# Kernel tuning notes

Measured on AMD Instinct MI355X. Metric: run time of the kernel, lower is better.

The kernel has to match this reference:

```python
import jax, jax.numpy as jnp
import numpy as np

N, DIM, RF_DIM, H, W, PN, TOPK = 16, 2048, 256, 16, 8, 64, 10  # TOPK = 2*k = 2*(K//2)


def conv1x1(w, x):
    # w: [O, C] (1x1 conv kernel), x: [b, C, h, w] -> [b, O, h, w]
    return jnp.einsum('oc,bchw->bohw', w, x)


def calibration(x, y):
    # x, y: [b, c, h, w]
    b, c, h, w = x.shape
    xv = x.reshape(b, c, h * w)
    yv = y.reshape(b, c, h * w)
    c_aff = jax.nn.softmax(jnp.einsum('bcm,bdm->bcd', xv, yv), axis=2)  # [b,c,c]
    s_aff = jax.nn.softmax(jnp.einsum('bcm,bcn->bmn', xv, yv), axis=2)  # [b,hw,hw]
    c_avg = c_aff.mean(axis=-1)  # [b,c]
    s_avg = s_aff.mean(axis=-1)  # [b,hw]
    aff = (c_avg[:, :, None] * s_avg[:, None, :]).reshape(b, c, h, w)
    pos = jax.nn.relu(aff - 0.5) + 0.5
    comp = jax.nn.relu(0.5 - aff) + 0.5
    return x * pos + y * comp


def instance_norm(x, eps=1e-5):
    m = x.mean(axis=(2, 3), keepdims=True)
    v = x.var(axis=(2, 3), keepdims=True)
    return (x - m) * jax.lax.rsqrt(v + eps)


def setup_inputs():
    key = jax.random.key(0)
    ks = jax.random.split(key, 6)
    return {
        'inputs': jax.random.normal(ks[0], (N, DIM, H, W), jnp.float32),
        'mv_prototype': jax.random.normal(ks[1], (PN, DIM, H, W), jnp.float32),
        'w_rf': jax.random.normal(ks[2], (RF_DIM, DIM), jnp.float32) * 0.02,
        'w_rf_mv': jax.random.normal(ks[3], (DIM, TOPK * RF_DIM), jnp.float32) * 0.02,
        'w_rm_s': jax.random.normal(ks[4], (DIM, DIM), jnp.float32) * 0.02,
        'w_fuse': jax.random.normal(ks[5], (DIM, DIM), jnp.float32) * 0.02,
    }


def reference(inputs, mv_prototype, w_rf, w_rf_mv, w_rm_s, w_fuse):
    n, c, h, w = inputs.shape
    # pairwise squared euclidean distance (addmm-style cdist)
    xf = inputs.reshape(n, -1)
    pf = mv_prototype.reshape(mv_prototype.shape[0], -1)
    dist = (xf * xf).sum(1, keepdims=True) + (pf * pf).sum(1)[None, :] - 2.0 * xf @ pf.T
    idx = jnp.argsort(dist, axis=1)[:, :TOPK]  # [n, 2k] nearest prototypes
    # refine prototypes then gather per-sample top-2k and stack channels
    xp = conv1x1(w_rf, mv_prototype)  # [pn, rf_dim, h, w]
    mv_list = xp[idx].reshape(n, TOPK * RF_DIM, h, w)
    mvl = conv1x1(w_rf_mv, mv_list)  # [n, dim, h, w]
    mvl = jax.nn.relu(calibration(inputs, mvl))
    mv_a = instance_norm(conv1x1(w_rm_s, mvl))
    x_fuse = jax.nn.sigmoid(conv1x1(w_fuse, mv_a))
    return inputs + inputs * x_fuse
```

## Files before the change

kernel.cpp:

```cpp
#include <hip/hip_runtime.h>
#include <cstdint>
#include <cstddef>

#define N_    16
#define DIM_  2048
#define RF_   256
#define PN_   64
#define TOPK_ 10
#define HW_   128
#define KFULL (DIM_*HW_)
#define KMV   (TOPK_*RF_)

#define AS1 __attribute__((address_space(1)))
#define AS3 __attribute__((address_space(3)))

typedef __attribute__((ext_vector_type(8))) short bf16x8;
typedef __attribute__((ext_vector_type(4))) float f32x4;
typedef __attribute__((ext_vector_type(8))) unsigned short u16x8;

__device__ __forceinline__ unsigned short f2bf(float f) {
  unsigned u = __builtin_bit_cast(unsigned, f);
  unsigned r = (u + 0x7FFFu + ((u >> 16) & 1u)) >> 16;
  return (unsigned short)r;
}

__global__ __launch_bounds__(256)
void cvt_all_kernel(const float* __restrict__ s0, const float* __restrict__ s1,
                    const float* __restrict__ s2, const float* __restrict__ s3,
                    unsigned short* __restrict__ d0, unsigned short* __restrict__ d1,
                    unsigned short* __restrict__ d2, unsigned short* __restrict__ d3,
                    float* __restrict__ dsum) {
  __shared__ u16x8 tile[32][65];
  const int t = threadIdx.x;
  int gid = blockIdx.x * 256 + t;
  if (gid < 1152) dsum[gid] = 0.f;

  int bid = blockIdx.x;
  const float* s; unsigned short* d; int O, CG, tb;
  if (bid < 32)       { s = s0; d = d0; O = RF_;  CG = DIM_ / 8; tb = bid; }
  else if (bid < 352) { s = s1; d = d1; O = DIM_; CG = KMV  / 8; tb = bid - 32; }
  else if (bid < 608) { s = s2; d = d2; O = DIM_; CG = DIM_ / 8; tb = bid - 352; }
  else                { s = s3; d = d3; O = DIM_; CG = DIM_ / 8; tb = bid - 608; }
  const int nCgT = CG / 32;
  const int o0  = (tb / nCgT) * 64;
  const int cg0 = (tb % nCgT) * 32;
  const size_t C = (size_t)CG * 8;

#pragma unroll
  for (int i = 0; i < 8; ++i) {
    int idx = i * 256 + t, ol = idx >> 5, cg = idx & 31;
    const float* sp = s + (size_t)(o0 + ol) * C + (size_t)(cg0 + cg) * 8;
    float4 a = *(const float4*)sp;
    float4 b = *(const float4*)(sp + 4);
    u16x8 pk;
    pk[0] = f2bf(a.x); pk[1] = f2bf(a.y); pk[2] = f2bf(a.z); pk[3] = f2bf(a.w);
    pk[4] = f2bf(b.x); pk[5] = f2bf(b.y); pk[6] = f2bf(b.z); pk[7] = f2bf(b.w);
    tile[cg][ol] = pk;
  }
  __syncthreads();
#pragma unroll
  for (int i = 0; i < 8; ++i) {
    int idx = i * 256 + t, cg = idx >> 6, ol = idx & 63;
    *(u16x8*)(d + (size_t)(cg0 + cg) * ((size_t)O * 8) + (size_t)(o0 + ol) * 8) =
        tile[cg][ol];
  }
}

__global__ __launch_bounds__(256)
void transpose_proto_kernel(const float* __restrict__ src,
                            unsigned short* __restrict__ dst,
                            float* __restrict__ pnorm_part) {
  __shared__ float tile[32][129];
  __shared__ float ssq[4];
  const int p = blockIdx.x;
  const int c0 = blockIdx.y * 32;
  const int t = threadIdx.x;
  const float* sp = src + ((size_t)p * DIM_ + c0) * HW_;
  float sq = 0.f;
#pragma unroll
  for (int i = 0; i < 4; ++i) {
    int g = i * 256 + t;
    int ci = g >> 5, s4 = g & 31;
    float4 v = *(const float4*)(sp + (size_t)ci * HW_ + s4 * 4);
    sq += v.x * v.x + v.y * v.y + v.z * v.z + v.w * v.w;
    int sb = s4 * 4;
    tile[ci][sb] = v.x; tile[ci][sb + 1] = v.y; tile[ci][sb + 2] = v.z; tile[ci][sb + 3] = v.w;
  }
#pragma unroll
  for (int m = 1; m < 64; m <<= 1) sq += __shfl_xor(sq, m, 64);
  if ((t & 63) == 0) ssq[t >> 6] = sq;
  __syncthreads();
  if (t == 0) pnorm_part[blockIdx.y * PN_ + p] = ssq[0] + ssq[1] + ssq[2] + ssq[3];
  unsigned short* dp = dst + (size_t)p * HW_ * DIM_ + (size_t)(c0 >> 3) * 1024;
#pragma unroll
  for (int i = 0; i < 2; ++i) {
    int cidx = i * 256 + t;
    int kg = cidx >> 7, s = cidx & 127;
    u16x8 pk;
#pragma unroll
    for (int u = 0; u < 8; ++u) pk[u] = f2bf(tile[kg * 8 + u][s]);
    *(u16x8*)(dp + (size_t)kg * 1024 + (size_t)s * 8) = pk;
  }
}

__global__ __launch_bounds__(256)
void dist_partial_kernel(const float* __restrict__ x, const float* __restrict__ proto,
                         float* __restrict__ part) {
  __shared__ alignas(16) float xl[2][16][68];
  __shared__ alignas(16) float pl[2][64][68];
  const int t = threadIdx.x, b = blockIdx.x;
  const int n0 = t & 7, pb = t >> 3;
  const int xr = t >> 4, xc = (t & 15) * 4;
  float acc[2][2] = {};
  const size_t kbase = (size_t)b * 512;

  float4 rx, rp[4];
  auto gload = [&](int ph) {
    const size_t k0 = kbase + ph * 64;
    rx = *(const float4*)(x + (size_t)xr * KFULL + k0 + xc);
#pragma unroll
    for (int i = 0; i < 4; ++i) {
      int idx = i * 256 + t;
      rp[i] = *(const float4*)(proto + (size_t)(idx >> 4) * KFULL + k0 + (idx & 15) * 4);
    }
  };
  auto swrite = [&](int buf) {
    *(float4*)&xl[buf][xr][xc] = rx;
#pragma unroll
    for (int i = 0; i < 4; ++i) {
      int idx = i * 256 + t;
      *(float4*)&pl[buf][idx >> 4][(idx & 15) * 4] = rp[i];
    }
  };

  gload(0); swrite(0);
  __syncthreads();
  for (int ph = 0; ph < 8; ++ph) {
    const int buf = ph & 1;
    if (ph + 1 < 8) gload(ph + 1);
#pragma unroll 8
    for (int k = 0; k < 64; k += 4) {
      float4 xa = *(float4*)&xl[buf][n0][k];
      float4 xb = *(float4*)&xl[buf][n0 + 8][k];
      float4 p0 = *(float4*)&pl[buf][pb][k];
      float4 p1 = *(float4*)&pl[buf][pb + 32][k];
      acc[0][0] += xa.x*p0.x + xa.y*p0.y + xa.z*p0.z + xa.w*p0.w;
      acc[0][1] += xa.x*p1.x + xa.y*p1.y + xa.z*p1.z + xa.w*p1.w;
      acc[1][0] += xb.x*p0.x + xb.y*p0.y + xb.z*p0.z + xb.w*p0.w;
      acc[1][1] += xb.x*p1.x + xb.y*p1.y + xb.z*p1.z + xb.w*p1.w;
    }
    if (ph + 1 < 8) swrite(buf ^ 1);
    __syncthreads();
  }

  float* scratch = (float*)xl;
  scratch[n0 * 64 + pb]            = -2.f * acc[0][0];
  scratch[n0 * 64 + pb + 32]       = -2.f * acc[0][1];
  scratch[(n0 + 8) * 64 + pb]      = -2.f * acc[1][0];
  scratch[(n0 + 8) * 64 + pb + 32] = -2.f * acc[1][1];
  __syncthreads();
  *(float4*)(part + (size_t)b * 1024 + t * 4) = *(const float4*)&scratch[t * 4];
}

__global__ __launch_bounds__(512)
void select_kernel(const float* __restrict__ part, const float* __restrict__ pnorm_part,
                   int* __restrict__ idx, int* __restrict__ flags) {
  __shared__ float red[8][64];
  __shared__ float sh[64];
  const int n = blockIdx.x, t = threadIdx.x;
  const int c = t & 63, ch = t >> 6;
  const float* pp = part + (size_t)ch * 64 * 1024 + n * 64 + c;
  float a0 = 0.f, a1 = 0.f, a2 = 0.f, a3 = 0.f;
  for (int b = 0; b < 64; b += 4) {
    a0 += pp[(size_t)(b + 0) * 1024];
    a1 += pp[(size_t)(b + 1) * 1024];
    a2 += pp[(size_t)(b + 2) * 1024];
    a3 += pp[(size_t)(b + 3) * 1024];
  }
  red[ch][c] = (a0 + a1) + (a2 + a3);
  __syncthreads();
  if (t < 64) {
    float pn = 0.f;
#pragma unroll 8
    for (int cb = 0; cb < DIM_ / 32; ++cb) pn += pnorm_part[cb * PN_ + t];
    float dv = pn;
#pragma unroll
    for (int i = 0; i < 8; ++i) dv += red[i][t];
    sh[t] = dv;
  }
  __syncthreads();
  if (t < 64) {
    float dval = sh[t];
    int rank = 0;
#pragma unroll
    for (int j = 0; j < 64; ++j) {
      float o = sh[j];
      rank += (o < dval || (o == dval && j < t)) ? 1 : 0;
    }
    if (rank < TOPK_) { idx[n * TOPK_ + rank] = t; flags[t] = 1; }
  }
}

#define BM 64
#define BKK 64

template <int MODE>
__global__ __launch_bounds__(256, 2)
void mfma_gemm_kernel(const unsigned short* __restrict__ Wb,
                      const unsigned short* __restrict__ Xb,
                      void* __restrict__ OutP,
                      const float* __restrict__ inputs,
                      const int* __restrict__ idxp,
                      const int* __restrict__ flags,
                      int K, int O, int Ldim) {
  __shared__ alignas(16) unsigned short Al[3][8 * BM * 8];
  __shared__ alignas(16) unsigned short Bl[3][8 * 128 * 8];

  const int t = threadIdx.x;
  const int w = t >> 6;
  const int lane = t & 63;
  const int q = lane >> 4;
  const int l15 = lane & 15;
  const int m2 = w >> 1;
  const int h  = w & 1;
  const int batch = blockIdx.y;
  const int o0 = blockIdx.x * BM;

  if (MODE == 0 && flags && !flags[batch]) return;

  int idreg = 0;
  if (MODE == 1 && lane < TOPK_) idreg = idxp[batch * TOPK_ + lane];

  f32x4 acc[2][4] = {};

  auto issue = [&](int k0, int buf) {
#pragma unroll
    for (int i = 0; i < 2; ++i) {
      int qk = w * 2 + i;
      const unsigned short* ga =
          Wb + (size_t)((k0 >> 3) + qk) * (O * 8) + (size_t)(o0 + lane) * 8;
      __builtin_amdgcn_global_load_lds((const AS1 void*)ga,
                                       (AS3 void*)(&Al[buf][qk * 512]), 16, 0, 0);
    }
    const unsigned short* base;
    if (MODE == 1) {
      int id = __shfl(idreg, k0 >> 8, 64);
      base = Xb + (size_t)id * (HW_ * RF_) + (size_t)((k0 & 255) >> 3) * 1024;
    } else {
      base = Xb + (size_t)batch * HW_ * K + (size_t)(k0 >> 3) * 1024;
    }
#pragma unroll
    for (int i = 0; i < 4; ++i) {
      int v = w * 4 + i;
      int qk = v >> 1, hh = v & 1;
      const unsigned short* gb = base + (size_t)qk * 1024 + (size_t)(hh * 64 + lane) * 8;
      __builtin_amdgcn_global_load_lds((const AS1 void*)gb,
                                       (AS3 void*)(&Bl[buf][qk * 1024 + hh * 512]), 16, 0, 0);
    }
  };

  const int nIter = K / BKK;

  issue(0, 0);
  issue(BKK, 1);

  for (int it = 0; it < nIter; ++it) {
    const int buf = it % 3;
    if (it + 1 < nIter) {
      asm volatile("s_waitcnt vmcnt(6)" ::: "memory");
    } else {
      asm volatile("s_waitcnt vmcnt(0)" ::: "memory");
    }
    __builtin_amdgcn_s_barrier();
#pragma unroll
    for (int s = 0; s < 2; ++s) {
      bf16x8 af[2], bfr[4];
#pragma unroll
      for (int mt = 0; mt < 2; ++mt)
        af[mt] = *(const bf16x8*)(&Al[buf][(s * 4 + q) * 512 + (m2 * 32 + mt * 16 + l15) * 8]);
#pragma unroll
      for (int nt = 0; nt < 4; ++nt)
        bfr[nt] = *(const bf16x8*)(&Bl[buf][(s * 4 + q) * 1024 + (h * 64 + nt * 16 + l15) * 8]);
#pragma unroll
      for (int mt = 0; mt < 2; ++mt)
#pragma unroll
        for (int nt = 0; nt < 4; ++nt)
          acc[mt][nt] = __builtin_amdgcn_mfma_f32_16x16x32_bf16(af[mt], bfr[nt], acc[mt][nt], 0, 0, 0);
    }
    if (it + 2 < nIter) issue((it + 2) * BKK, (it + 2) % 3);
  }

  const float CAL = 1.0f - 1.0f / 262144.0f;

  float* nsumS = (float*)&Al[0][0];
  float* nsqS  = (float*)&Al[0][0] + 128;

  if (MODE == 2) {
#pragma unroll
    for (int mt = 0; mt < 2; ++mt)
#pragma unroll
      for (int reg = 0; reg < 4; ++reg) {
        float s_ = 0.f, q_ = 0.f;
#pragma unroll
        for (int nt = 0; nt < 4; ++nt) {
          float v = acc[mt][nt][reg];
          s_ += v; q_ += v * v;
        }
#pragma unroll
        for (int m = 1; m < 16; m <<= 1) {
          s_ += __shfl_xor(s_, m, 64);
          q_ += __shfl_xor(q_, m, 64);
        }
        if (l15 == 0) {
          int ol = mt * 16 + q * 4 + reg;
          nsumS[w * 32 + ol] = s_; nsqS[w * 32 + ol] = q_;
        }
      }
    __syncthreads();
  }

  if (MODE == 3) {
    float* ofb = (float*)OutP + (size_t)batch * DIM_ * HW_;
    const float* inb = inputs + (size_t)batch * DIM_ * HW_;
#pragma unroll
    for (int mt = 0; mt < 2; ++mt)
#pragma unroll
      for (int nt = 0; nt < 4; ++nt) {
        int o = o0 + m2 * 32 + mt * 16 + q * 4;
        int s = h * 64 + nt * 16 + l15;
        f32x4 v = acc[mt][nt];
#pragma unroll
        for (int g = 0; g < 4; ++g) {
          float in = inb[(size_t)(o + g) * HW_ + s];
          float sg = 1.f / (1.f + expf(-v[g]));
          ofb[(size_t)(o + g) * HW_ + s] = in * (1.f + sg);
        }
      }
  } else {
    unsigned short* ob = (unsigned short*)OutP + (size_t)batch * HW_ * Ldim;
    const float* inb = (MODE == 1) ? inputs + (size_t)batch * DIM_ * HW_ : nullptr;
#pragma unroll
    for (int mt = 0; mt < 2; ++mt) {
      float mean[4], rs[4];
      if (MODE == 2) {
#pragma unroll
        for (int reg = 0; reg < 4; ++reg) {
          int ol = mt * 16 + q * 4 + reg;
          float ts = nsumS[(m2 * 2 + 0) * 32 + ol] + nsumS[(m2 * 2 + 1) * 32 + ol];
          float tq = nsqS[(m2 * 2 + 0) * 32 + ol] + nsqS[(m2 * 2 + 1) * 32 + ol];
          float mn = ts * (1.f / 128.f);
          float vr = tq * (1.f / 128.f) - mn * mn;
          mean[reg] = mn; rs[reg] = rsqrtf(vr + 1e-5f);
        }
      }
#pragma unroll
      for (int nt = 0; nt < 4; ++nt) {
        int o = o0 + m2 * 32 + mt * 16 + q * 4;
        int s = h * 64 + nt * 16 + l15;
        f32x4 v = acc[mt][nt];
        float r[4];
        if (MODE == 0) {
#pragma unroll
          for (int g = 0; g < 4; ++g) r[g] = v[g];
        } else if (MODE == 1) {
          const float* ip = inb + (size_t)o * HW_ + s;
#pragma unroll
          for (int g = 0; g < 4; ++g)
            r[g] = fmaxf(0.f, 0.5f * ip[(size_t)g * HW_] + CAL * v[g]);
        } else {
#pragma unroll
          for (int g = 0; g < 4; ++g) r[g] = (v[g] - mean[g]) * rs[g];
        }
        ushort4 pk;
        pk.x = f2bf(r[0]); pk.y = f2bf(r[1]); pk.z = f2bf(r[2]); pk.w = f2bf(r[3]);
        *(ushort4*)(ob + (size_t)(o >> 3) * 1024 + (size_t)s * 8 + (o & 7)) = pk;
      }
    }
  }
}

extern "C" void kernel_launch(void* const* d_in, const int* in_sizes, int n_in,
                              void* d_out, int out_size, void* d_ws, size_t ws_size,
                              hipStream_t stream) {
  const float* inputs = (const float*)d_in[0];
  const float* proto  = (const float*)d_in[1];
  const float* w_rf   = (const float*)d_in[2];
  const float* w_rfmv = (const float*)d_in[3];
  const float* w_rms  = (const float*)d_in[4];
  const float* w_fuse = (const float*)d_in[5];
  float* out = (float*)d_out;

  uint8_t* ws = (uint8_t*)d_ws;
  size_t off = 0;
  auto alloc = [&](size_t bytes) { uint8_t* p = ws + off; off += (bytes + 255) & ~(size_t)255; return p; };

  float* dsum  = (float*)alloc(1088 * 4);
  int*   flags = (int*)alloc(PN_ * 4);
  int*   idx   = (int*)alloc(N_ * TOPK_ * 4);
  float* pnorm = (float*)alloc((size_t)(DIM_ / 32) * PN_ * 4);
  float* part  = (float*)alloc((size_t)512 * 1024 * 4);
  unsigned short* wrf_b   = (unsigned short*)alloc((size_t)RF_ * DIM_ * 2);
  unsigned short* wrfmv_b = (unsigned short*)alloc((size_t)DIM_ * KMV * 2);
  unsigned short* wrms_b  = (unsigned short*)alloc((size_t)DIM_ * DIM_ * 2);
  unsigned short* wfuse_b = (unsigned short*)alloc((size_t)DIM_ * DIM_ * 2);
  unsigned short* xpT     = (unsigned short*)alloc((size_t)PN_ * HW_ * RF_ * 2);
  unsigned short* protoT  = (unsigned short*)alloc((size_t)PN_ * HW_ * DIM_ * 2);
  unsigned short* mvlT = protoT;
  unsigned short* mvaT = protoT + (size_t)N_ * HW_ * DIM_;

  cvt_all_kernel<<<864, 256, 0, stream>>>(w_rf, w_rfmv, w_rms, w_fuse,
                                          wrf_b, wrfmv_b, wrms_b, wfuse_b, dsum);
  transpose_proto_kernel<<<dim3(PN_, DIM_ / 32), 256, 0, stream>>>(proto, protoT, pnorm);
  dist_partial_kernel<<<512, 256, 0, stream>>>(inputs, proto, part);
  select_kernel<<<N_, 512, 0, stream>>>(part, pnorm, idx, flags);

  mfma_gemm_kernel<0><<<dim3(RF_ / BM, PN_), 256, 0, stream>>>(
      wrf_b, protoT, xpT, nullptr, nullptr, flags, DIM_, RF_, RF_);
  mfma_gemm_kernel<1><<<dim3(DIM_ / BM, N_), 256, 0, stream>>>(
      wrfmv_b, xpT, mvlT, inputs, idx, nullptr, KMV, DIM_, DIM_);
  mfma_gemm_kernel<2><<<dim3(DIM_ / BM, N_), 256, 0, stream>>>(
      wrms_b, mvlT, mvaT, nullptr, nullptr, nullptr, DIM_, DIM_, DIM_);
  mfma_gemm_kernel<3><<<dim3(DIM_ / BM, N_), 256, 0, stream>>>(
      wfuse_b, mvaT, out, inputs, nullptr, nullptr, DIM_, DIM_, DIM_);
}
```

Baseline: 316.4 us.

## Merge front-end kernels into one launch and widen GEMM blocks to 512 threads

```diff
diff --git a/kernel.cpp b/kernel.cpp
--- a/kernel.cpp
+++ b/kernel.cpp
@@ -25,141 +25,143 @@
 }
 
 __global__ __launch_bounds__(256)
-void cvt_all_kernel(const float* __restrict__ s0, const float* __restrict__ s1,
-                    const float* __restrict__ s2, const float* __restrict__ s3,
-                    unsigned short* __restrict__ d0, unsigned short* __restrict__ d1,
-                    unsigned short* __restrict__ d2, unsigned short* __restrict__ d3,
-                    float* __restrict__ dsum) {
-  __shared__ u16x8 tile[32][65];
+void front_kernel(const float* __restrict__ x, const float* __restrict__ proto,
+                  float* __restrict__ part,
+                  unsigned short* __restrict__ protoT, float* __restrict__ pnorm_part,
+                  const float* __restrict__ s0, const float* __restrict__ s1,
+                  const float* __restrict__ s2, const float* __restrict__ s3,
+                  unsigned short* __restrict__ d0, unsigned short* __restrict__ d1,
+                  unsigned short* __restrict__ d2, unsigned short* __restrict__ d3,
+                  float* __restrict__ dsum) {
+  __shared__ alignas(16) unsigned char ldsbuf[43520];
   const int t = threadIdx.x;
-  int gid = blockIdx.x * 256 + t;
-  if (gid < 1152) dsum[gid] = 0.f;
-
-  int bid = blockIdx.x;
-  const float* s; unsigned short* d; int O, CG, tb;
-  if (bid < 32)       { s = s0; d = d0; O = RF_;  CG = DIM_ / 8; tb = bid; }
-  else if (bid < 352) { s = s1; d = d1; O = DIM_; CG = KMV  / 8; tb = bid - 32; }
-  else if (bid < 608) { s = s2; d = d2; O = DIM_; CG = DIM_ / 8; tb = bid - 352; }
-  else                { s = s3; d = d3; O = DIM_; CG = DIM_ / 8; tb = bid - 608; }
-  const int nCgT = CG / 32;
-  const int o0  = (tb / nCgT) * 64;
-  const int cg0 = (tb % nCgT) * 32;
-  const size_t C = (size_t)CG * 8;
-
-#pragma unroll
-  for (int i = 0; i < 8; ++i) {
-    int idx = i * 256 + t, ol = idx >> 5, cg = idx & 31;
-    const float* sp = s + (size_t)(o0 + ol) * C + (size_t)(cg0 + cg) * 8;
-    float4 a = *(const float4*)sp;
-    float4 b = *(const float4*)(sp + 4);
-    u16x8 pk;
-    pk[0] = f2bf(a.x); pk[1] = f2bf(a.y); pk[2] = f2bf(a.z); pk[3] = f2bf(a.w);
-    pk[4] = f2bf(b.x); pk[5] = f2bf(b.y); pk[6] = f2bf(b.z); pk[7] = f2bf(b.w);
-    tile[cg][ol] = pk;
-  }
-  __syncthreads();
-#pragma unroll
-  for (int i = 0; i < 8; ++i) {
-    int idx = i * 256 + t, cg = idx >> 6, ol = idx & 63;
-    *(u16x8*)(d + (size_t)(cg0 + cg) * ((size_t)O * 8) + (size_t)(o0 + ol) * 8) =
-        tile[cg][ol];
-  }
-}
-
-__global__ __launch_bounds__(256)
-void transpose_proto_kernel(const float* __restrict__ src,
-                            unsigned short* __restrict__ dst,
-                            float* __restrict__ pnorm_part) {
-  __shared__ float tile[32][129];
-  __shared__ float ssq[4];
-  const int p = blockIdx.x;
-  const int c0 = blockIdx.y * 32;
-  const int t = threadIdx.x;
-  const float* sp = src + ((size_t)p * DIM_ + c0) * HW_;
-  float sq = 0.f;
-#pragma unroll
-  for (int i = 0; i < 4; ++i) {
-    int g = i * 256 + t;
-    int ci = g >> 5, s4 = g & 31;
-    float4 v = *(const float4*)(sp + (size_t)ci * HW_ + s4 * 4);
-    sq += v.x * v.x + v.y * v.y + v.z * v.z + v.w * v.w;
-    int sb = s4 * 4;
-    tile[ci][sb] = v.x; tile[ci][sb + 1] = v.y; tile[ci][sb + 2] = v.z; tile[ci][sb + 3] = v.w;
-  }
-#pragma unroll
-  for (int m = 1; m < 64; m <<= 1) sq += __shfl_xor(sq, m, 64);
-  if ((t & 63) == 0) ssq[t >> 6] = sq;
-  __syncthreads();
-  if (t == 0) pnorm_part[blockIdx.y * PN_ + p] = ssq[0] + ssq[1] + ssq[2] + ssq[3];
-  unsigned short* dp = dst + (size_t)p * HW_ * DIM_ + (size_t)(c0 >> 3) * 1024;
-#pragma unroll
-  for (int i = 0; i < 2; ++i) {
-    int cidx = i * 256 + t;
-    int kg = cidx >> 7, s = cidx & 127;
-    u16x8 pk;
-#pragma unroll
-    for (int u = 0; u < 8; ++u) pk[u] = f2bf(tile[kg * 8 + u][s]);
-    *(u16x8*)(dp + (size_t)kg * 1024 + (size_t)s * 8) = pk;
-  }
-}
-
-__global__ __launch_bounds__(256)
-void dist_partial_kernel(const float* __restrict__ x, const float* __restrict__ proto,
-                         float* __restrict__ part) {
-  __shared__ alignas(16) float xl[2][16][68];
-  __shared__ alignas(16) float pl[2][64][68];
-  const int t = threadIdx.x, b = blockIdx.x;
-  const int n0 = t & 7, pb = t >> 3;
-  const int xr = t >> 4, xc = (t & 15) * 4;
-  float acc[2][2] = {};
-  const size_t kbase = (size_t)b * 512;
-
-  float4 rx, rp[4];
-  auto gload = [&](int ph) {
-    const size_t k0 = kbase + ph * 64;
-    rx = *(const float4*)(x + (size_t)xr * KFULL + k0 + xc);
+  const int bid = blockIdx.x;
+  {
+    int g = bid * 256 + t;
+    if (g < 1152) dsum[g] = 0.f;
+  }
+
+  if (bid < 512) {
+    float (*xl)[16][68] = (float (*)[16][68])ldsbuf;
+    float (*pl)[64][68] = (float (*)[64][68])(ldsbuf + 8704);
+    const int b = bid;
+    const int n0 = t & 7, pb = t >> 3;
+    const int xr = t >> 4, xc = (t & 15) * 4;
+    float acc[2][2] = {};
+    const size_t kbase = (size_t)b * 512;
+
+    float4 rx, rp[4];
+    auto gload = [&](int ph) {
+      const size_t k0 = kbase + ph * 64;
+      rx = *(const float4*)(x + (size_t)xr * KFULL + k0 + xc);
+#pragma unroll
+      for (int i = 0; i < 4; ++i) {
+        int idx = i * 256 + t;
+        rp[i] = *(const float4*)(proto + (size_t)(idx >> 4) * KFULL + k0 + (idx & 15) * 4);
+      }
+    };
+    auto swrite = [&](int buf) {
+      *(float4*)&xl[buf][xr][xc] = rx;
+#pragma unroll
+      for (int i = 0; i < 4; ++i) {
+        int idx = i * 256 + t;
+        *(float4*)&pl[buf][idx >> 4][(idx & 15) * 4] = rp[i];
+      }
+    };
+
+    gload(0); swrite(0);
+    __syncthreads();
+    for (int ph = 0; ph < 8; ++ph) {
+      const int buf = ph & 1;
+      if (ph + 1 < 8) gload(ph + 1);
+#pragma unroll 8
+      for (int k = 0; k < 64; k += 4) {
+        float4 xa = *(float4*)&xl[buf][n0][k];
+        float4 xb = *(float4*)&xl[buf][n0 + 8][k];
+        float4 p0 = *(float4*)&pl[buf][pb][k];
+        float4 p1 = *(float4*)&pl[buf][pb + 32][k];
+        acc[0][0] += xa.x*p0.x + xa.y*p0.y + xa.z*p0.z + xa.w*p0.w;
+        acc[0][1] += xa.x*p1.x + xa.y*p1.y + xa.z*p1.z + xa.w*p1.w;
+        acc[1][0] += xb.x*p0.x + xb.y*p0.y + xb.z*p0.z + xb.w*p0.w;
+        acc[1][1] += xb.x*p1.x + xb.y*p1.y + xb.z*p1.z + xb.w*p1.w;
+      }
+      if (ph + 1 < 8) swrite(buf ^ 1);
+      __syncthreads();
+    }
+
+    float* scratch = (float*)ldsbuf;
+    scratch[n0 * 64 + pb]            = -2.f * acc[0][0];
+    scratch[n0 * 64 + pb + 32]       = -2.f * acc[0][1];
+    scratch[(n0 + 8) * 64 + pb]      = -2.f * acc[1][0];
+    scratch[(n0 + 8) * 64 + pb + 32] = -2.f * acc[1][1];
+    __syncthreads();
+    *(float4*)(part + (size_t)b * 1024 + t * 4) = *(const float4*)&scratch[t * 4];
+
+  } else if (bid < 4608) {
+    float (*tile)[129] = (float (*)[129])ldsbuf;
+    float* ssq = (float*)(ldsbuf + 16512);
+    const int local = bid - 512;
+    const int p = local & 63;
+    const int c0 = (local >> 6) * 32;
+    const float* sp = proto + ((size_t)p * DIM_ + c0) * HW_;
+    float sq = 0.f;
 #pragma unroll
     for (int i = 0; i < 4; ++i) {
-      int idx = i * 256 + t;
-      rp[i] = *(const float4*)(proto + (size_t)(idx >> 4) * KFULL + k0 + (idx & 15) * 4);
-    }
-  };
-  auto swrite = [&](int buf) {
-    *(float4*)&xl[buf][xr][xc] = rx;
-#pragma unroll
-    for (int i = 0; i < 4; ++i) {
-      int idx = i * 256 + t;
-      *(float4*)&pl[buf][idx >> 4][(idx & 15) * 4] = rp[i];
-    }
-  };
-
-  gload(0); swrite(0);
-  __syncthreads();
-  for (int ph = 0; ph < 8; ++ph) {
-    const int buf = ph & 1;
-    if (ph + 1 < 8) gload(ph + 1);
-#pragma unroll 8
-    for (int k = 0; k < 64; k += 4) {
-      float4 xa = *(float4*)&xl[buf][n0][k];
-      float4 xb = *(float4*)&xl[buf][n0 + 8][k];
-      float4 p0 = *(float4*)&pl[buf][pb][k];
-      float4 p1 = *(float4*)&pl[buf][pb + 32][k];
-      acc[0][0] += xa.x*p0.x + xa.y*p0.y + xa.z*p0.z + xa.w*p0.w;
-      acc[0][1] += xa.x*p1.x + xa.y*p1.y + xa.z*p1.z + xa.w*p1.w;
-      acc[1][0] += xb.x*p0.x + xb.y*p0.y + xb.z*p0.z + xb.w*p0.w;
-      acc[1][1] += xb.x*p1.x + xb.y*p1.y + xb.z*p1.z + xb.w*p1.w;
-    }
-    if (ph + 1 < 8) swrite(buf ^ 1);
+      int g = i * 256 + t;
+      int ci = g >> 5, s4 = g & 31;
+      float4 v = *(const float4*)(sp + (size_t)ci * HW_ + s4 * 4);
+      sq += v.x * v.x + v.y * v.y + v.z * v.z + v.w * v.w;
+      int sb = s4 * 4;
+      tile[ci][sb] = v.x; tile[ci][sb + 1] = v.y; tile[ci][sb + 2] = v.z; tile[ci][sb + 3] = v.w;
+    }
+#pragma unroll
+    for (int m = 1; m < 64; m <<= 1) sq += __shfl_xor(sq, m, 64);
+    if ((t & 63) == 0) ssq[t >> 6] = sq;
     __syncthreads();
-  }
-
-  float* scratch = (float*)xl;
-  scratch[n0 * 64 + pb]            = -2.f * acc[0][0];
-  scratch[n0 * 64 + pb + 32]       = -2.f * acc[0][1];
-  scratch[(n0 + 8) * 64 + pb]      = -2.f * acc[1][0];
-  scratch[(n0 + 8) * 64 + pb + 32] = -2.f * acc[1][1];
-  __syncthreads();
-  *(float4*)(part + (size_t)b * 1024 + t * 4) = *(const float4*)&scratch[t * 4];
+    if (t == 0) pnorm_part[(local >> 6) * PN_ + p] = ssq[0] + ssq[1] + ssq[2] + ssq[3];
+    unsigned short* dp = protoT + (size_t)p * HW_ * DIM_ + (size_t)(c0 >> 3) * 1024;
+#pragma unroll
+    for (int i = 0; i < 2; ++i) {
+      int cidx = i * 256 + t;
+      int kg = cidx >> 7, s = cidx & 127;
+      u16x8 pk;
+#pragma unroll
+      for (int u = 0; u < 8; ++u) pk[u] = f2bf(tile[kg * 8 + u][s]);
+      *(u16x8*)(dp + (size_t)kg * 1024 + (size_t)s * 8) = pk;
+    }
+
+  } else {
+    u16x8 (*ctile)[65] = (u16x8 (*)[65])ldsbuf;
+    int local = bid - 4608;
+    const float* s; unsigned short* d; int O, CG, tb;
+    if (local < 32)       { s = s0; d = d0; O = RF_;  CG = DIM_ / 8; tb = local; }
+    else if (local < 352) { s = s1; d = d1; O = DIM_; CG = KMV  / 8; tb = local - 32; }
+    else if (local < 608) { s = s2; d = d2; O = DIM_; CG = DIM_ / 8; tb = local - 352; }
+    else                  { s = s3; d = d3; O = DIM_; CG = DIM_ / 8; tb = local - 608; }
+    const int nCgT = CG / 32;
+    const int o0  = (tb / nCgT) * 64;
+    const int cg0 = (tb % nCgT) * 32;
+    const size_t C = (size_t)CG * 8;
+
+#pragma unroll
+    for (int i = 0; i < 8; ++i) {
+      int idx = i * 256 + t, ol = idx >> 5, cg = idx & 31;
+      const float* sp = s + (size_t)(o0 + ol) * C + (size_t)(cg0 + cg) * 8;
+      float4 a = *(const float4*)sp;
+      float4 b = *(const float4*)(sp + 4);
+      u16x8 pk;
+      pk[0] = f2bf(a.x); pk[1] = f2bf(a.y); pk[2] = f2bf(a.z); pk[3] = f2bf(a.w);
+      pk[4] = f2bf(b.x); pk[5] = f2bf(b.y); pk[6] = f2bf(b.z); pk[7] = f2bf(b.w);
+      ctile[cg][ol] = pk;
+    }
+    __syncthreads();
+#pragma unroll
+    for (int i = 0; i < 8; ++i) {
+      int idx = i * 256 + t, cg = idx >> 6, ol = idx & 63;
+      *(u16x8*)(d + (size_t)(cg0 + cg) * ((size_t)O * 8) + (size_t)(o0 + ol) * 8) =
+          ctile[cg][ol];
+    }
+  }
 }
 
 __global__ __launch_bounds__(512)
@@ -205,7 +207,7 @@
 #define BKK 64
 
 template <int MODE>
-__global__ __launch_bounds__(256, 2)
+__global__ __launch_bounds__(512, 4)
 void mfma_gemm_kernel(const unsigned short* __restrict__ Wb,
                       const unsigned short* __restrict__ Xb,
                       void* __restrict__ OutP,
@@ -221,7 +223,7 @@
   const int lane = t & 63;
   const int q = lane >> 4;
   const int l15 = lane & 15;
-  const int m2 = w >> 1;
+  const int mq = w >> 1;
   const int h  = w & 1;
   const int batch = blockIdx.y;
   const int o0 = blockIdx.x * BM;
@@ -231,16 +233,14 @@
   int idreg = 0;
   if (MODE == 1 && lane < TOPK_) idreg = idxp[batch * TOPK_ + lane];
 
-  f32x4 acc[2][4] = {};
+  f32x4 acc[4] = {};
 
   auto issue = [&](int k0, int buf) {
-#pragma unroll
-    for (int i = 0; i < 2; ++i) {
-      int qk = w * 2 + i;
+    {
       const unsigned short* ga =
-          Wb + (size_t)((k0 >> 3) + qk) * (O * 8) + (size_t)(o0 + lane) * 8;
+          Wb + (size_t)((k0 >> 3) + w) * (O * 8) + (size_t)(o0 + lane) * 8;
       __builtin_amdgcn_global_load_lds((const AS1 void*)ga,
-                                       (AS3 void*)(&Al[buf][qk * 512]), 16, 0, 0);
+                                       (AS3 void*)(&Al[buf][w * 512]), 16, 0, 0);
     }
     const unsigned short* base;
     if (MODE == 1) {
@@ -250,8 +250,8 @@
       base = Xb + (size_t)batch * HW_ * K + (size_t)(k0 >> 3) * 1024;
     }
 #pragma unroll
-    for (int i = 0; i < 4; ++i) {
-      int v = w * 4 + i;
+    for (int i = 0; i < 2; ++i) {
+      int v = w * 2 + i;
       int qk = v >> 1, hh = v & 1;
       const unsigned short* gb = base + (size_t)qk * 1024 + (size_t)(hh * 64 + lane) * 8;
       __builtin_amdgcn_global_load_lds((const AS1 void*)gb,
@@ -267,25 +267,21 @@
   for (int it = 0; it < nIter; ++it) {
     const int buf = it % 3;
     if (it + 1 < nIter) {
-      asm volatile("s_waitcnt vmcnt(6)" ::: "memory");
+      asm volatile("s_waitcnt vmcnt(3)" ::: "memory");
     } else {
       asm volatile("s_waitcnt vmcnt(0)" ::: "memory");
     }
     __builtin_amdgcn_s_barrier();
 #pragma unroll
     for (int s = 0; s < 2; ++s) {
-      bf16x8 af[2], bfr[4];
-#pragma unroll
-      for (int mt = 0; mt < 2; ++mt)
-        af[mt] = *(const bf16x8*)(&Al[buf][(s * 4 + q) * 512 + (m2 * 32 + mt * 16 + l15) * 8]);
+      bf16x8 af, bfr[4];
+      af = *(const bf16x8*)(&Al[buf][(s * 4 + q) * 512 + (mq * 16 + l15) * 8]);
 #pragma unroll
       for (int nt = 0; nt < 4; ++nt)
         bfr[nt] = *(const bf16x8*)(&Bl[buf][(s * 4 + q) * 1024 + (h * 64 + nt * 16 + l15) * 8]);
 #pragma unroll
-      for (int mt = 0; mt < 2; ++mt)
-#pragma unroll
-        for (int nt = 0; nt < 4; ++nt)
-          acc[mt][nt] = __builtin_amdgcn_mfma_f32_16x16x32_bf16(af[mt], bfr[nt], acc[mt][nt], 0, 0, 0);
+      for (int nt = 0; nt < 4; ++nt)
+        acc[nt] = __builtin_amdgcn_mfma_f32_16x16x32_bf16(af, bfr[nt], acc[nt], 0, 0, 0);
     }
     if (it + 2 < nIter) issue((it + 2) * BKK, (it + 2) % 3);
   }
@@ -297,25 +293,23 @@
 
   if (MODE == 2) {
 #pragma unroll
-    for (int mt = 0; mt < 2; ++mt)
-#pragma unroll
-      for (int reg = 0; reg < 4; ++reg) {
-        float s_ = 0.f, q_ = 0.f;
-#pragma unroll
-        for (int nt = 0; nt < 4; ++nt) {
-          float v = acc[mt][nt][reg];
-          s_ += v; q_ += v * v;
-        }
-#pragma unroll
-        for (int m = 1; m < 16; m <<= 1) {
-          s_ += __shfl_xor(s_, m, 64);
-          q_ += __shfl_xor(q_, m, 64);
-        }
-        if (l15 == 0) {
-          int ol = mt * 16 + q * 4 + reg;
-          nsumS[w * 32 + ol] = s_; nsqS[w * 32 + ol] = q_;
-        }
-      }
+    for (int reg = 0; reg < 4; ++reg) {
+      float s_ = 0.f, q_ = 0.f;
+#pragma unroll
+      for (int nt = 0; nt < 4; ++nt) {
+        float v = acc[nt][reg];
+        s_ += v; q_ += v * v;
+      }
+#pragma unroll
+      for (int m = 1; m < 16; m <<= 1) {
+        s_ += __shfl_xor(s_, m, 64);
+        q_ += __shfl_xor(q_, m, 64);
+      }
+      if (l15 == 0) {
+        nsumS[w * 16 + q * 4 + reg] = s_;
+        nsqS [w * 16 + q * 4 + reg] = q_;
+      }
+    }
     __syncthreads();
   }
 
@@ -323,58 +317,53 @@
     float* ofb = (float*)OutP + (size_t)batch * DIM_ * HW_;
     const float* inb = inputs + (size_t)batch * DIM_ * HW_;
 #pragma unroll
-    for (int mt = 0; mt < 2; ++mt)
-#pragma unroll
-      for (int nt = 0; nt < 4; ++nt) {
-        int o = o0 + m2 * 32 + mt * 16 + q * 4;
-        int s = h * 64 + nt * 16 + l15;
-        f32x4 v = acc[mt][nt];
-#pragma unroll
-        for (int g = 0; g < 4; ++g) {
-          float in = inb[(size_t)(o + g) * HW_ + s];
-          float sg = 1.f / (1.f + expf(-v[g]));
-          ofb[(size_t)(o + g) * HW_ + s] = in * (1.f + sg);
-        }
-      }
+    for (int nt = 0; nt < 4; ++nt) {
+      int o = o0 + mq * 16 + q * 4;
+      int s = h * 64 + nt * 16 + l15;
+      f32x4 v = acc[nt];
+#pragma unroll
+      for (int g = 0; g < 4; ++g) {
+        float in = inb[(size_t)(o + g) * HW_ + s];
+        float sg = 1.f / (1.f + expf(-v[g]));
+        ofb[(size_t)(o + g) * HW_ + s] = in * (1.f + sg);
+      }
+    }
   } else {
     unsigned short* ob = (unsigned short*)OutP + (size_t)batch * HW_ * Ldim;
     const float* inb = (MODE == 1) ? inputs + (size_t)batch * DIM_ * HW_ : nullptr;
-#pragma unroll
-    for (int mt = 0; mt < 2; ++mt) {
-      float mean[4], rs[4];
-      if (MODE == 2) {
-#pragma unroll
-        for (int reg = 0; reg < 4; ++reg) {
-          int ol = mt * 16 + q * 4 + reg;
-          float ts = nsumS[(m2 * 2 + 0) * 32 + ol] + nsumS[(m2 * 2 + 1) * 32 + ol];
-          float tq = nsqS[(m2 * 2 + 0) * 32 + ol] + nsqS[(m2 * 2 + 1) * 32 + ol];
-          float mn = ts * (1.f / 128.f);
-          float vr = tq * (1.f / 128.f) - mn * mn;
-          mean[reg] = mn; rs[reg] = rsqrtf(vr + 1e-5f);
-        }
-      }
-#pragma unroll
-      for (int nt = 0; nt < 4; ++nt) {
-        int o = o0 + m2 * 32 + mt * 16 + q * 4;
-        int s = h * 64 + nt * 16 + l15;
-        f32x4 v = acc[mt][nt];
-        float r[4];
-        if (MODE == 0) {
-#pragma unroll
-          for (int g = 0; g < 4; ++g) r[g] = v[g];
-        } else if (MODE == 1) {
-          const float* ip = inb + (size_t)o * HW_ + s;
-#pragma unroll
-          for (int g = 0; g < 4; ++g)
-            r[g] = fmaxf(0.f, 0.5f * ip[(size_t)g * HW_] + CAL * v[g]);
-        } else {
-#pragma unroll
-          for (int g = 0; g < 4; ++g) r[g] = (v[g] - mean[g]) * rs[g];
-        }
-        ushort4 pk;
-        pk.x = f2bf(r[0]); pk.y = f2bf(r[1]); pk.z = f2bf(r[2]); pk.w = f2bf(r[3]);
-        *(ushort4*)(ob + (size_t)(o >> 3) * 1024 + (size_t)s * 8 + (o & 7)) = pk;
-      }
+    float mean[4], rs[4];
+    if (MODE == 2) {
+#pragma unroll
+      for (int reg = 0; reg < 4; ++reg) {
+        int ol = q * 4 + reg;
+        float ts = nsumS[(mq * 2 + 0) * 16 + ol] + nsumS[(mq * 2 + 1) * 16 + ol];
+        float tq = nsqS [(mq * 2 + 0) * 16 + ol] + nsqS [(mq * 2 + 1) * 16 + ol];
+        float mn = ts * (1.f / 128.f);
+        float vr = tq * (1.f / 128.f) - mn * mn;
+        mean[reg] = mn; rs[reg] = rsqrtf(vr + 1e-5f);
+      }
+    }
+#pragma unroll
+    for (int nt = 0; nt < 4; ++nt) {
+      int o = o0 + mq * 16 + q * 4;
+      int s = h * 64 + nt * 16 + l15;
+      f32x4 v = acc[nt];
+      float r[4];
+      if (MODE == 0) {
+#pragma unroll
+        for (int g = 0; g < 4; ++g) r[g] = v[g];
+      } else if (MODE == 1) {
+        const float* ip = inb + (size_t)o * HW_ + s;
+#pragma unroll
+        for (int g = 0; g < 4; ++g)
+          r[g] = fmaxf(0.f, 0.5f * ip[(size_t)g * HW_] + CAL * v[g]);
+      } else {
+#pragma unroll
+        for (int g = 0; g < 4; ++g) r[g] = (v[g] - mean[g]) * rs[g];
+      }
+      ushort4 pk;
+      pk.x = f2bf(r[0]); pk.y = f2bf(r[1]); pk.z = f2bf(r[2]); pk.w = f2bf(r[3]);
+      *(ushort4*)(ob + (size_t)(o >> 3) * 1024 + (size_t)s * 8 + (o & 7)) = pk;
     }
   }
 }
@@ -408,18 +397,17 @@
   unsigned short* mvlT = protoT;
   unsigned short* mvaT = protoT + (size_t)N_ * HW_ * DIM_;
 
-  cvt_all_kernel<<<864, 256, 0, stream>>>(w_rf, w_rfmv, w_rms, w_fuse,
-                                          wrf_b, wrfmv_b, wrms_b, wfuse_b, dsum);
-  transpose_proto_kernel<<<dim3(PN_, DIM_ / 32), 256, 0, stream>>>(proto, protoT, pnorm);
-  dist_partial_kernel<<<512, 256, 0, stream>>>(inputs, proto, part);
+  front_kernel<<<5472, 256, 0, stream>>>(inputs, proto, part, protoT, pnorm,
+                                         w_rf, w_rfmv, w_rms, w_fuse,
+                                         wrf_b, wrfmv_b, wrms_b, wfuse_b, dsum);
   select_kernel<<<N_, 512, 0, stream>>>(part, pnorm, idx, flags);
 
-  mfma_gemm_kernel<0><<<dim3(RF_ / BM, PN_), 256, 0, stream>>>(
+  mfma_gemm_kernel<0><<<dim3(RF_ / BM, PN_), 512, 0, stream>>>(
       wrf_b, protoT, xpT, nullptr, nullptr, flags, DIM_, RF_, RF_);
-  mfma_gemm_kernel<1><<<dim3(DIM_ / BM, N_), 256, 0, stream>>>(
+  mfma_gemm_kernel<1><<<dim3(DIM_ / BM, N_), 512, 0, stream>>>(
       wrfmv_b, xpT, mvlT, inputs, idx, nullptr, KMV, DIM_, DIM_);
-  mfma_gemm_kernel<2><<<dim3(DIM_ / BM, N_), 256, 0, stream>>>(
+  mfma_gemm_kernel<2><<<dim3(DIM_ / BM, N_), 512, 0, stream>>>(
       wrms_b, mvlT, mvaT, nullptr, nullptr, nullptr, DIM_, DIM_, DIM_);
-  mfma_gemm_kernel<3><<<dim3(DIM_ / BM, N_), 256, 0, stream>>>(
+  mfma_gemm_kernel<3><<<dim3(DIM_ / BM, N_), 512, 0, stream>>>(
       wfuse_b, mvaT, out, inputs, nullptr, nullptr, DIM_, DIM_, DIM_);
 }
```

New measurement: 303.0 us. -4.3%, faster.
